# Kernel tuning notes

Hardware: AMD Instinct MI355X
Metric: run time of the kernel (lower is better)

Reference implementation:

```python
import jax, jax.numpy as jnp
import numpy as np

D_MODEL = 256
N_HEADS = 8
N_LEVELS = 3
N_POINTS = 4
HEAD_DIM = D_MODEL // N_HEADS
SPATIAL_SHAPES = [(80, 80), (40, 40), (20, 20)]
B = 16
LEN_Q = 300
N_TOTAL = sum(h * w for h, w in SPATIAL_SHAPES)  # 8400
N_LP = N_LEVELS * N_POINTS


def setup_inputs() -> dict:
    key = jax.random.key(0)
    ks = jax.random.split(key, 8)
    s = 0.02
    return {
        "query": jax.random.normal(ks[0], (B, LEN_Q, D_MODEL), jnp.float32),
        "reference_points": jax.random.uniform(ks[1], (B, LEN_Q, N_LEVELS, 2), jnp.float32),
        "input_flatten": jax.random.normal(ks[2], (B, N_TOTAL, D_MODEL), jnp.float32),
        "W_off": jax.random.normal(ks[3], (D_MODEL, N_HEADS * N_LP * 2), jnp.float32) * s,
        "b_off": jnp.zeros((N_HEADS * N_LP * 2,), jnp.float32),
        "W_attn": jax.random.normal(ks[4], (D_MODEL, N_HEADS * N_LP), jnp.float32) * s,
        "b_attn": jnp.zeros((N_HEADS * N_LP,), jnp.float32),
        "W_val": jax.random.normal(ks[5], (D_MODEL, D_MODEL), jnp.float32) * s,
        "b_val": jnp.zeros((D_MODEL,), jnp.float32),
        "W_out": jax.random.normal(ks[6], (D_MODEL, D_MODEL), jnp.float32) * s,
        "b_out": jnp.zeros((D_MODEL,), jnp.float32),
    }


def _ms_deform_core(value, sampling_locations, attention_weights):
    # value: (B, n_heads, head_dim, N_total); locations: (B, Lq, H, L, P, 2) in [0,1]
    Bq, Lq = sampling_locations.shape[0], sampling_locations.shape[1]
    BN = Bq * N_HEADS
    grids = 2.0 * sampling_locations - 1.0
    starts = np.cumsum([0] + [h * w for h, w in SPATIAL_SHAPES])
    sampled_levels = []
    for lid, (H, W) in enumerate(SPATIAL_SHAPES):
        val_l = value[..., starts[lid]:starts[lid + 1]]                    # (B,H,hd,HW)
        val_flat = val_l.reshape(BN, HEAD_DIM, H * W).transpose(0, 2, 1)   # (BN,HW,hd)
        g = grids[:, :, :, lid].transpose(0, 2, 1, 3, 4).reshape(BN, Lq, N_POINTS, 2)
        ix = ((g[..., 0] + 1.0) * W - 1.0) / 2.0
        iy = ((g[..., 1] + 1.0) * H - 1.0) / 2.0
        ix0 = jnp.floor(ix).astype(jnp.int32)
        iy0 = jnp.floor(iy).astype(jnp.int32)
        ix1 = ix0 + 1
        iy1 = iy0 + 1
        fx = (ix - ix0.astype(ix.dtype))[..., None]
        fy = (iy - iy0.astype(iy.dtype))[..., None]

        def corner(iyc, ixc):
            valid = ((ixc >= 0) & (ixc < W) & (iyc >= 0) & (iyc < H)).astype(val_flat.dtype)
            idx = (jnp.clip(iyc, 0, H - 1) * W + jnp.clip(ixc, 0, W - 1))
            idx = idx.reshape(BN, Lq * N_POINTS, 1)
            v = jnp.take_along_axis(val_flat, idx, axis=1)
            return v.reshape(BN, Lq, N_POINTS, HEAD_DIM) * valid[..., None]

        v00 = corner(iy0, ix0)
        v01 = corner(iy0, ix1)
        v10 = corner(iy1, ix0)
        v11 = corner(iy1, ix1)
        sampled = ((1 - fx) * (1 - fy)) * v00 + (fx * (1 - fy)) * v01 \
                + ((1 - fx) * fy) * v10 + (fx * fy) * v11
        sampled_levels.append(sampled.transpose(0, 3, 1, 2))               # (BN,hd,Lq,P)
    sv = jnp.stack(sampled_levels, axis=-2).reshape(BN, HEAD_DIM, Lq, N_LP)
    a = attention_weights.transpose(0, 2, 1, 3).reshape(BN, 1, Lq, N_LP)
    out = jnp.sum(sv * a, axis=-1)                                         # (BN,hd,Lq)
    return out.reshape(Bq, D_MODEL, Lq).transpose(0, 2, 1)                 # (B,Lq,D)


def reference(query, reference_points, input_flatten,
              W_off, b_off, W_attn, b_attn, W_val, b_val, W_out, b_out):
    Bq, Lq = query.shape[0], query.shape[1]
    value = input_flatten @ W_val + b_val
    value = value.reshape(Bq, -1, N_HEADS, HEAD_DIM).transpose(0, 2, 3, 1)  # (B,H,hd,N)
    off = (query @ W_off + b_off).reshape(Bq, Lq, N_HEADS, N_LEVELS, N_POINTS, 2)
    attn = jax.nn.softmax((query @ W_attn + b_attn).reshape(Bq, Lq, N_HEADS, N_LP), axis=-1)
    # offset normalizer is (W,H) per level (x first)
    norm = jnp.array([[w, h] for h, w in SPATIAL_SHAPES], jnp.float32)
    loc = reference_points[:, :, None, :, None, :] + off / norm[None, None, None, :, None, :]
    out = _ms_deform_core(value, loc, attn)
    return out @ W_out + b_out
```

## Files before the change

kernel.cpp:

```cpp
#include <hip/hip_runtime.h>
#include <hip/hip_bf16.h>

#define DM 256
#define NH 8
#define HD 32
#define NLV 3
#define NPT 4
#define NLP 12
#define BB 16
#define LQ 300
#define NT 8400
#define MROWS (BB * NT)
#define QROWS (BB * LQ)
#define KP 40

typedef __bf16 bf16x8 __attribute__((ext_vector_type(8)));
typedef __bf16 bf16x4 __attribute__((ext_vector_type(4)));
typedef float  f32x16 __attribute__((ext_vector_type(16)));

__global__ void k_wt(const float* __restrict__ W_val,
                     const float* __restrict__ W_off,
                     const float* __restrict__ W_attn,
                     const float* __restrict__ W_out,
                     __hip_bfloat16* __restrict__ Wt,
                     __hip_bfloat16* __restrict__ Wt2,
                     __hip_bfloat16* __restrict__ Wt3)
{
    const int n = blockIdx.x;
    const int k = threadIdx.x;
    if (n < 256) {
        Wt[(size_t)(k >> 5) * 8192 + n * 32 + (k & 31)] =
            __float2bfloat16(W_val[(size_t)k * 256 + n]);
    } else if (n < 544) {
        const int n2 = n - 256;
        float v = (n2 < 192) ? W_off[(size_t)k * 192 + n2]
                             : W_attn[(size_t)k * 96 + (n2 - 192)];
        Wt2[(size_t)(k >> 5) * 9216 + n2 * 32 + (k & 31)] = __float2bfloat16(v);
    } else {
        const int n3 = n - 544;
        Wt3[(size_t)(k >> 5) * 8192 + n3 * 32 + (k & 31)] =
            __float2bfloat16(W_out[(size_t)k * 256 + n3]);
    }
}

__global__ __launch_bounds__(256) void k_valproj(
    const float* __restrict__ A,
    const __hip_bfloat16* __restrict__ Wt,
    const float* __restrict__ bias,
    __hip_bfloat16* __restrict__ V)
{
    __shared__ __hip_bfloat16 As[2][64 * KP];
    __shared__ __hip_bfloat16 Ws[2][256 * KP];

    const int t    = threadIdx.x;
    const int m0   = blockIdx.x * 64;
    const int wave = t >> 6;
    const int lane = t & 63;
    const int lm   = lane & 31;
    const int lk   = (lane >> 5) * 8;

    f32x16 acc[2][2];
#pragma unroll
    for (int i = 0; i < 2; i++)
#pragma unroll
        for (int j = 0; j < 2; j++)
#pragma unroll
            for (int e = 0; e < 16; e++) acc[i][j][e] = 0.f;

    const int ar = t >> 2;
    const int ak = (t & 3) * 8;

    float4 a0, a1;
    bf16x8 w0, w1, w2, w3;

    {
        const float* ap = A + (size_t)(m0 + ar) * 256 + ak;
        a0 = *(const float4*)ap;
        a1 = *(const float4*)(ap + 4);
        const __hip_bfloat16* wp = Wt + t * 32;
        w0 = *(const bf16x8*)(wp + 0);
        w1 = *(const bf16x8*)(wp + 8);
        w2 = *(const bf16x8*)(wp + 16);
        w3 = *(const bf16x8*)(wp + 24);
    }
    {
        union { __hip_bfloat162 h2[4]; bf16x8 v; } ua;
        ua.h2[0] = __float22bfloat162_rn(make_float2(a0.x, a0.y));
        ua.h2[1] = __float22bfloat162_rn(make_float2(a0.z, a0.w));
        ua.h2[2] = __float22bfloat162_rn(make_float2(a1.x, a1.y));
        ua.h2[3] = __float22bfloat162_rn(make_float2(a1.z, a1.w));
        *(bf16x8*)(&As[0][ar * KP + ak]) = ua.v;
        __hip_bfloat16* wd = &Ws[0][t * KP];
        *(bf16x8*)(wd + 0)  = w0;
        *(bf16x8*)(wd + 8)  = w1;
        *(bf16x8*)(wd + 16) = w2;
        *(bf16x8*)(wd + 24) = w3;
    }
    __syncthreads();

    for (int it = 0; it < 8; ++it) {
        float4 na0, na1;
        bf16x8 nw0, nw1, nw2, nw3;
        if (it < 7) {
            const int kt = (it + 1) * 32;
            const float* ap = A + (size_t)(m0 + ar) * 256 + kt + ak;
            na0 = *(const float4*)ap;
            na1 = *(const float4*)(ap + 4);
            const __hip_bfloat16* wp = Wt + (size_t)(it + 1) * 8192 + t * 32;
            nw0 = *(const bf16x8*)(wp + 0);
            nw1 = *(const bf16x8*)(wp + 8);
            nw2 = *(const bf16x8*)(wp + 16);
            nw3 = *(const bf16x8*)(wp + 24);
        }
        const int buf = it & 1;
#pragma unroll
        for (int kk = 0; kk < 32; kk += 16) {
            bf16x8 af0 = *(const bf16x8*)(&As[buf][(0 * 32 + lm) * KP + kk + lk]);
            bf16x8 af1 = *(const bf16x8*)(&As[buf][(1 * 32 + lm) * KP + kk + lk]);
            bf16x8 bf0 = *(const bf16x8*)(&Ws[buf][(wave * 64 + 0 * 32 + lm) * KP + kk + lk]);
            bf16x8 bf1 = *(const bf16x8*)(&Ws[buf][(wave * 64 + 1 * 32 + lm) * KP + kk + lk]);
            acc[0][0] = __builtin_amdgcn_mfma_f32_32x32x16_bf16(af0, bf0, acc[0][0], 0, 0, 0);
            acc[0][1] = __builtin_amdgcn_mfma_f32_32x32x16_bf16(af0, bf1, acc[0][1], 0, 0, 0);
            acc[1][0] = __builtin_amdgcn_mfma_f32_32x32x16_bf16(af1, bf0, acc[1][0], 0, 0, 0);
            acc[1][1] = __builtin_amdgcn_mfma_f32_32x32x16_bf16(af1, bf1, acc[1][1], 0, 0, 0);
        }
        if (it < 7) {
            union { __hip_bfloat162 h2[4]; bf16x8 v; } ua;
            ua.h2[0] = __float22bfloat162_rn(make_float2(na0.x, na0.y));
            ua.h2[1] = __float22bfloat162_rn(make_float2(na0.z, na0.w));
            ua.h2[2] = __float22bfloat162_rn(make_float2(na1.x, na1.y));
            ua.h2[3] = __float22bfloat162_rn(make_float2(na1.z, na1.w));
            const int nb = buf ^ 1;
            *(bf16x8*)(&As[nb][ar * KP + ak]) = ua.v;
            __hip_bfloat16* wd = &Ws[nb][t * KP];
            *(bf16x8*)(wd + 0)  = nw0;
            *(bf16x8*)(wd + 8)  = nw1;
            *(bf16x8*)(wd + 16) = nw2;
            *(bf16x8*)(wd + 24) = nw3;
            __syncthreads();
        }
    }

#pragma unroll
    for (int ni = 0; ni < 2; ni++) {
        const int n  = wave * 64 + ni * 32 + lm;
        const float bn = bias[n];
        const int h  = n >> 5;
        const int d  = n & 31;
#pragma unroll
        for (int mi = 0; mi < 2; mi++) {
#pragma unroll
            for (int r = 0; r < 16; r++) {
                int rl = (r & 3) + 8 * (r >> 2) + 4 * (lane >> 5);
                int m  = m0 + mi * 32 + rl;
                int b  = m / NT;
                int pos = m - b * NT;
                V[((size_t)(b * NH + h) * NT + pos) * HD + d] =
                    __float2bfloat16(acc[mi][ni][r] + bn);
            }
        }
    }
}

__global__ __launch_bounds__(192) void k_offattn(
    const float* __restrict__ Q,
    const __hip_bfloat16* __restrict__ Wt2,
    const float* __restrict__ boff,
    const float* __restrict__ battn,
    float* __restrict__ off_out,
    float* __restrict__ attn_out)
{
    __shared__ __hip_bfloat16 As[32 * KP];
    __shared__ __hip_bfloat16 Ws[288 * KP];

    const int t    = threadIdx.x;
    const int m0   = blockIdx.x * 32;
    const int wave = t >> 6;
    const int lane = t & 63;
    const int lm   = lane & 31;
    const int lk   = (lane >> 5) * 8;

    f32x16 acc[3];
#pragma unroll
    for (int j = 0; j < 3; j++)
#pragma unroll
        for (int e = 0; e < 16; e++) acc[j][e] = 0.f;

    for (int kt = 0; kt < 256; kt += 32) {
        if (t < 128) {
            const int ar = t >> 2;
            const int ak = (t & 3) * 8;
            const float* ap = Q + (size_t)(m0 + ar) * 256 + kt + ak;
            float4 a0 = *(const float4*)ap;
            float4 a1 = *(const float4*)(ap + 4);
            union { __hip_bfloat162 h2[4]; bf16x8 v; } ua;
            ua.h2[0] = __float22bfloat162_rn(make_float2(a0.x, a0.y));
            ua.h2[1] = __float22bfloat162_rn(make_float2(a0.z, a0.w));
            ua.h2[2] = __float22bfloat162_rn(make_float2(a1.x, a1.y));
            ua.h2[3] = __float22bfloat162_rn(make_float2(a1.z, a1.w));
            *(bf16x8*)(As + ar * KP + ak) = ua.v;
        }
        {
            const __hip_bfloat16* wp = Wt2 + (size_t)(kt >> 5) * 9216 + t * 32;
            __hip_bfloat16* wd = Ws + t * KP;
            *(bf16x8*)(wd + 0)  = *(const bf16x8*)(wp + 0);
            *(bf16x8*)(wd + 8)  = *(const bf16x8*)(wp + 8);
            *(bf16x8*)(wd + 16) = *(const bf16x8*)(wp + 16);
            *(bf16x8*)(wd + 24) = *(const bf16x8*)(wp + 24);
            if (t < 96) {
                const __hip_bfloat16* wp2 = Wt2 + (size_t)(kt >> 5) * 9216 + (t + 192) * 32;
                __hip_bfloat16* wd2 = Ws + (t + 192) * KP;
                *(bf16x8*)(wd2 + 0)  = *(const bf16x8*)(wp2 + 0);
                *(bf16x8*)(wd2 + 8)  = *(const bf16x8*)(wp2 + 8);
                *(bf16x8*)(wd2 + 16) = *(const bf16x8*)(wp2 + 16);
                *(bf16x8*)(wd2 + 24) = *(const bf16x8*)(wp2 + 24);
            }
        }
        __syncthreads();

#pragma unroll
        for (int kk = 0; kk < 32; kk += 16) {
            bf16x8 af = *(const bf16x8*)(As + lm * KP + kk + lk);
#pragma unroll
            for (int j = 0; j < 3; j++) {
                bf16x8 bf = *(const bf16x8*)(Ws + (wave * 96 + j * 32 + lm) * KP + kk + lk);
                acc[j] = __builtin_amdgcn_mfma_f32_32x32x16_bf16(af, bf, acc[j], 0, 0, 0);
            }
        }
        __syncthreads();
    }

#pragma unroll
    for (int j = 0; j < 3; j++) {
        const int n = wave * 96 + j * 32 + lm;
        const float bias_ = (n < 192) ? boff[n] : battn[n - 192];
#pragma unroll
        for (int r = 0; r < 16; r++) {
            int rl = (r & 3) + 8 * (r >> 2) + 4 * (lane >> 5);
            int m  = m0 + rl;
            float v = acc[j][r] + bias_;
            if (n < 192) off_out[(size_t)m * 192 + n] = v;
            else         attn_out[(size_t)m * 96 + (n - 192)] = v;
        }
    }
}

__global__ __launch_bounds__(256) void k_sample(
    const float* __restrict__ off_raw,
    const float* __restrict__ attn_raw,
    const float* __restrict__ refp,
    const __hip_bfloat16* __restrict__ V,
    __hip_bfloat16* __restrict__ sampled)
{
    const int t  = threadIdx.x;
    const int q2 = t >> 7;
    const int tq = t & 127;
    const int bq = blockIdx.x * 2 + q2;
    const int b  = bq / LQ;

    __shared__ float aw[2][96];
    __shared__ float wc[2][96][4];
    __shared__ int   ic[2][96][4];

    if (tq < 8) {
        float v[12];
        float mx = -1e30f;
#pragma unroll
        for (int i = 0; i < 12; i++) {
            v[i] = attn_raw[(size_t)bq * 96 + tq * 12 + i];
            mx = fmaxf(mx, v[i]);
        }
        float s = 0.f;
#pragma unroll
        for (int i = 0; i < 12; i++) { v[i] = expf(v[i] - mx); s += v[i]; }
        float inv = 1.f / s;
#pragma unroll
        for (int i = 0; i < 12; i++) aw[q2][tq * 12 + i] = v[i] * inv;
    }
    __syncthreads();

    if (tq < 96) {
        const float dims[3]  = {80.f, 40.f, 20.f};
        const int startsl[3] = {0, 6400, 8000};
        const int idiml[3]   = {80, 40, 20};
        int h = tq / 12, lp = tq - h * 12, l = lp >> 2, p = lp & 3;
        float ox = off_raw[(size_t)bq * 192 + ((h * 3 + l) * 4 + p) * 2 + 0];
        float oy = off_raw[(size_t)bq * 192 + ((h * 3 + l) * 4 + p) * 2 + 1];
        float rx = refp[(size_t)bq * 6 + l * 2 + 0];
        float ry = refp[(size_t)bq * 6 + l * 2 + 1];
        float D  = dims[l];
        float lx = rx + ox / D;
        float ly = ry + oy / D;
        float ix = lx * D - 0.5f;
        float iy = ly * D - 0.5f;
        const int Dl = idiml[l];
        const int st = startsl[l];

        float fix = floorf(ix), fiy = floorf(iy);
        int ix0 = (int)fix, iy0 = (int)fiy;
        int ix1 = ix0 + 1, iy1 = iy0 + 1;
        float fx = ix - fix, fy = iy - fiy;

        float mx0 = (ix0 >= 0 && ix0 < Dl) ? 1.f : 0.f;
        float mx1 = (ix1 >= 0 && ix1 < Dl) ? 1.f : 0.f;
        float my0 = (iy0 >= 0 && iy0 < Dl) ? 1.f : 0.f;
        float my1 = (iy1 >= 0 && iy1 < Dl) ? 1.f : 0.f;

        int cx0 = min(max(ix0, 0), Dl - 1);
        int cx1 = min(max(ix1, 0), Dl - 1);
        int cy0 = min(max(iy0, 0), Dl - 1);
        int cy1 = min(max(iy1, 0), Dl - 1);

        float a = aw[q2][tq];
        wc[q2][tq][0] = (1.f - fx) * (1.f - fy) * mx0 * my0 * a;
        wc[q2][tq][1] = fx * (1.f - fy) * mx1 * my0 * a;
        wc[q2][tq][2] = (1.f - fx) * fy * mx0 * my1 * a;
        wc[q2][tq][3] = fx * fy * mx1 * my1 * a;
        ic[q2][tq][0] = (st + cy0 * Dl + cx0) * HD;
        ic[q2][tq][1] = (st + cy0 * Dl + cx1) * HD;
        ic[q2][tq][2] = (st + cy1 * Dl + cx0) * HD;
        ic[q2][tq][3] = (st + cy1 * Dl + cx1) * HD;
    }
    __syncthreads();

    const int h  = tq >> 4;
    const int dp = (tq & 15) * 2;
    const __hip_bfloat16* vb = V + (size_t)(b * NH + h) * NT * HD + dp;

    float acc0 = 0.f, acc1 = 0.f;
#pragma unroll
    for (int lp = 0; lp < 12; lp++) {
        const int s = h * 12 + lp;
        float4 w4 = *(const float4*)(&wc[q2][s][0]);
        int4   i4 = *(const int4*)(&ic[q2][s][0]);
        float2 v00 = __bfloat1622float2(*(const __hip_bfloat162*)(vb + i4.x));
        float2 v01 = __bfloat1622float2(*(const __hip_bfloat162*)(vb + i4.y));
        float2 v10 = __bfloat1622float2(*(const __hip_bfloat162*)(vb + i4.z));
        float2 v11 = __bfloat1622float2(*(const __hip_bfloat162*)(vb + i4.w));
        acc0 = fmaf(w4.x, v00.x, fmaf(w4.y, v01.x, fmaf(w4.z, v10.x, fmaf(w4.w, v11.x, acc0))));
        acc1 = fmaf(w4.x, v00.y, fmaf(w4.y, v01.y, fmaf(w4.z, v10.y, fmaf(w4.w, v11.y, acc1))));
    }
    *(__hip_bfloat162*)(sampled + (size_t)bq * 256 + h * 32 + dp) =
        __float22bfloat162_rn(make_float2(acc0, acc1));
}

__global__ __launch_bounds__(256) void k_outproj(
    const __hip_bfloat16* __restrict__ A,
    const __hip_bfloat16* __restrict__ Wt3,
    const float* __restrict__ bias,
    float* __restrict__ out)
{
    __shared__ __hip_bfloat16 As[32 * KP];
    __shared__ __hip_bfloat16 Ws[256 * KP];

    const int t    = threadIdx.x;
    const int m0   = blockIdx.x * 32;
    const int wave = t >> 6;
    const int lane = t & 63;
    const int lm   = lane & 31;
    const int lk   = (lane >> 5) * 8;

    f32x16 acc[2];
#pragma unroll
    for (int j = 0; j < 2; j++)
#pragma unroll
        for (int e = 0; e < 16; e++) acc[j][e] = 0.f;

    const int ar = t >> 3;
    const int ak = (t & 7) * 4;

    for (int kt = 0; kt < 256; kt += 32) {
        *(bf16x4*)(As + ar * KP + ak) =
            *(const bf16x4*)(A + (size_t)(m0 + ar) * 256 + kt + ak);
        {
            const __hip_bfloat16* wp = Wt3 + (size_t)(kt >> 5) * 8192 + t * 32;
            __hip_bfloat16* wd = Ws + t * KP;
            *(bf16x8*)(wd + 0)  = *(const bf16x8*)(wp + 0);
            *(bf16x8*)(wd + 8)  = *(const bf16x8*)(wp + 8);
            *(bf16x8*)(wd + 16) = *(const bf16x8*)(wp + 16);
            *(bf16x8*)(wd + 24) = *(const bf16x8*)(wp + 24);
        }
        __syncthreads();

#pragma unroll
        for (int kk = 0; kk < 32; kk += 16) {
            bf16x8 af = *(const bf16x8*)(As + lm * KP + kk + lk);
            bf16x8 bf0 = *(const bf16x8*)(Ws + (wave * 64 + 0 * 32 + lm) * KP + kk + lk);
            bf16x8 bf1 = *(const bf16x8*)(Ws + (wave * 64 + 1 * 32 + lm) * KP + kk + lk);
            acc[0] = __builtin_amdgcn_mfma_f32_32x32x16_bf16(af, bf0, acc[0], 0, 0, 0);
            acc[1] = __builtin_amdgcn_mfma_f32_32x32x16_bf16(af, bf1, acc[1], 0, 0, 0);
        }
        __syncthreads();
    }

#pragma unroll
    for (int j = 0; j < 2; j++) {
        const int n = wave * 64 + j * 32 + lm;
        const float bn = bias[n];
#pragma unroll
        for (int r = 0; r < 16; r++) {
            int rl = (r & 3) + 8 * (r >> 2) + 4 * (lane >> 5);
            int m  = m0 + rl;
            out[(size_t)m * 256 + n] = acc[j][r] + bn;
        }
    }
}

extern "C" void kernel_launch(void* const* d_in, const int* in_sizes, int n_in,
                              void* d_out, int out_size, void* d_ws, size_t ws_size,
                              hipStream_t stream) {
    const float* query  = (const float*)d_in[0];
    const float* refp   = (const float*)d_in[1];
    const float* inputf = (const float*)d_in[2];
    const float* W_off  = (const float*)d_in[3];
    const float* b_off  = (const float*)d_in[4];
    const float* W_attn = (const float*)d_in[5];
    const float* b_attn = (const float*)d_in[6];
    const float* W_val  = (const float*)d_in[7];
    const float* b_val  = (const float*)d_in[8];
    const float* W_out  = (const float*)d_in[9];
    const float* b_out  = (const float*)d_in[10];
    float* out = (float*)d_out;

    char* ws = (char*)d_ws;
    __hip_bfloat16* value   = (__hip_bfloat16*)ws;
    float* off_raw          = (float*)(ws + 68812800);
    float* attn_raw         = (float*)(ws + 72499200);
    __hip_bfloat16* sampled = (__hip_bfloat16*)(ws + 74342400);
    __hip_bfloat16* Wt      = (__hip_bfloat16*)(ws + 76800000);
    __hip_bfloat16* Wt2     = (__hip_bfloat16*)(ws + 76931072);
    __hip_bfloat16* Wt3     = (__hip_bfloat16*)(ws + 77078528);

    k_wt<<<800, 256, 0, stream>>>(W_val, W_off, W_attn, W_out, Wt, Wt2, Wt3);
    k_valproj<<<MROWS / 64, 256, 0, stream>>>(inputf, Wt, b_val, value);
    k_offattn<<<QROWS / 32, 192, 0, stream>>>(query, Wt2, b_off, b_attn,
                                              off_raw, attn_raw);
    k_sample<<<QROWS / 2, 256, 0, stream>>>(off_raw, attn_raw, refp, value, sampled);
    k_outproj<<<QROWS / 32, 256, 0, stream>>>(sampled, Wt3, b_out, out);
}
```

Before: 283.4 us.

## Restructure value projection GEMM to 32-row tiles with single-buffered K=64 stages

The value-projection kernel now handles 32 rows per block instead of 64, launching twice as many blocks. It also drops the register-prefetch double buffering in favour of a single LDS buffer that stages K in chunks of 64 with two barriers per chunk. The smaller per-block footprint is meant to raise occupancy and parallelism. In exchange, each block reuses the weight tile across fewer rows, so weight loads into LDS double, and global load latency is no longer overlapped with MFMA work.

```diff
diff --git a/kernel.cpp b/kernel.cpp
--- a/kernel.cpp
+++ b/kernel.cpp
@@ -13,6 +13,7 @@
 #define MROWS (BB * NT)
 #define QROWS (BB * LQ)
 #define KP 40
+#define KP2 72
 
 typedef __bf16 bf16x8 __attribute__((ext_vector_type(8)));
 typedef __bf16 bf16x4 __attribute__((ext_vector_type(4)));
@@ -49,115 +50,78 @@
     const float* __restrict__ bias,
     __hip_bfloat16* __restrict__ V)
 {
-    __shared__ __hip_bfloat16 As[2][64 * KP];
-    __shared__ __hip_bfloat16 Ws[2][256 * KP];
+    __shared__ __hip_bfloat16 As[32 * KP2];
+    __shared__ __hip_bfloat16 Ws[256 * KP2];
 
     const int t    = threadIdx.x;
-    const int m0   = blockIdx.x * 64;
+    const int m0   = blockIdx.x * 32;
     const int wave = t >> 6;
     const int lane = t & 63;
     const int lm   = lane & 31;
     const int lk   = (lane >> 5) * 8;
 
-    f32x16 acc[2][2];
-#pragma unroll
-    for (int i = 0; i < 2; i++)
-#pragma unroll
-        for (int j = 0; j < 2; j++)
-#pragma unroll
-            for (int e = 0; e < 16; e++) acc[i][j][e] = 0.f;
-
-    const int ar = t >> 2;
-    const int ak = (t & 3) * 8;
-
-    float4 a0, a1;
-    bf16x8 w0, w1, w2, w3;
-
-    {
-        const float* ap = A + (size_t)(m0 + ar) * 256 + ak;
-        a0 = *(const float4*)ap;
-        a1 = *(const float4*)(ap + 4);
-        const __hip_bfloat16* wp = Wt + t * 32;
-        w0 = *(const bf16x8*)(wp + 0);
-        w1 = *(const bf16x8*)(wp + 8);
-        w2 = *(const bf16x8*)(wp + 16);
-        w3 = *(const bf16x8*)(wp + 24);
-    }
-    {
-        union { __hip_bfloat162 h2[4]; bf16x8 v; } ua;
-        ua.h2[0] = __float22bfloat162_rn(make_float2(a0.x, a0.y));
-        ua.h2[1] = __float22bfloat162_rn(make_float2(a0.z, a0.w));
-        ua.h2[2] = __float22bfloat162_rn(make_float2(a1.x, a1.y));
-        ua.h2[3] = __float22bfloat162_rn(make_float2(a1.z, a1.w));
-        *(bf16x8*)(&As[0][ar * KP + ak]) = ua.v;
-        __hip_bfloat16* wd = &Ws[0][t * KP];
-        *(bf16x8*)(wd + 0)  = w0;
-        *(bf16x8*)(wd + 8)  = w1;
-        *(bf16x8*)(wd + 16) = w2;
-        *(bf16x8*)(wd + 24) = w3;
-    }
-    __syncthreads();
-
-    for (int it = 0; it < 8; ++it) {
-        float4 na0, na1;
-        bf16x8 nw0, nw1, nw2, nw3;
-        if (it < 7) {
-            const int kt = (it + 1) * 32;
+    f32x16 acc[2];
+#pragma unroll
+    for (int j = 0; j < 2; j++)
+#pragma unroll
+        for (int e = 0; e < 16; e++) acc[j][e] = 0.f;
+
+    const int ar = t >> 3;
+    const int ak = (t & 7) * 8;
+
+    for (int kt = 0; kt < 256; kt += 64) {
+        {
             const float* ap = A + (size_t)(m0 + ar) * 256 + kt + ak;
-            na0 = *(const float4*)ap;
-            na1 = *(const float4*)(ap + 4);
-            const __hip_bfloat16* wp = Wt + (size_t)(it + 1) * 8192 + t * 32;
-            nw0 = *(const bf16x8*)(wp + 0);
-            nw1 = *(const bf16x8*)(wp + 8);
-            nw2 = *(const bf16x8*)(wp + 16);
-            nw3 = *(const bf16x8*)(wp + 24);
-        }
-        const int buf = it & 1;
-#pragma unroll
-        for (int kk = 0; kk < 32; kk += 16) {
-            bf16x8 af0 = *(const bf16x8*)(&As[buf][(0 * 32 + lm) * KP + kk + lk]);
-            bf16x8 af1 = *(const bf16x8*)(&As[buf][(1 * 32 + lm) * KP + kk + lk]);
-            bf16x8 bf0 = *(const bf16x8*)(&Ws[buf][(wave * 64 + 0 * 32 + lm) * KP + kk + lk]);
-            bf16x8 bf1 = *(const bf16x8*)(&Ws[buf][(wave * 64 + 1 * 32 + lm) * KP + kk + lk]);
-            acc[0][0] = __builtin_amdgcn_mfma_f32_32x32x16_bf16(af0, bf0, acc[0][0], 0, 0, 0);
-            acc[0][1] = __builtin_amdgcn_mfma_f32_32x32x16_bf16(af0, bf1, acc[0][1], 0, 0, 0);
-            acc[1][0] = __builtin_amdgcn_mfma_f32_32x32x16_bf16(af1, bf0, acc[1][0], 0, 0, 0);
-            acc[1][1] = __builtin_amdgcn_mfma_f32_32x32x16_bf16(af1, bf1, acc[1][1], 0, 0, 0);
-        }
-        if (it < 7) {
+            float4 a0 = *(const float4*)ap;
+            float4 a1 = *(const float4*)(ap + 4);
             union { __hip_bfloat162 h2[4]; bf16x8 v; } ua;
-            ua.h2[0] = __float22bfloat162_rn(make_float2(na0.x, na0.y));
-            ua.h2[1] = __float22bfloat162_rn(make_float2(na0.z, na0.w));
-            ua.h2[2] = __float22bfloat162_rn(make_float2(na1.x, na1.y));
-            ua.h2[3] = __float22bfloat162_rn(make_float2(na1.z, na1.w));
-            const int nb = buf ^ 1;
-            *(bf16x8*)(&As[nb][ar * KP + ak]) = ua.v;
-            __hip_bfloat16* wd = &Ws[nb][t * KP];
-            *(bf16x8*)(wd + 0)  = nw0;
-            *(bf16x8*)(wd + 8)  = nw1;
-            *(bf16x8*)(wd + 16) = nw2;
-            *(bf16x8*)(wd + 24) = nw3;
-            __syncthreads();
-        }
-    }
-
-#pragma unroll
-    for (int ni = 0; ni < 2; ni++) {
-        const int n  = wave * 64 + ni * 32 + lm;
+            ua.h2[0] = __float22bfloat162_rn(make_float2(a0.x, a0.y));
+            ua.h2[1] = __float22bfloat162_rn(make_float2(a0.z, a0.w));
+            ua.h2[2] = __float22bfloat162_rn(make_float2(a1.x, a1.y));
+            ua.h2[3] = __float22bfloat162_rn(make_float2(a1.z, a1.w));
+            *(bf16x8*)(As + ar * KP2 + ak) = ua.v;
+        }
+        {
+            const int kt5 = kt >> 5;
+            const __hip_bfloat16* wp0 = Wt + (size_t)kt5 * 8192 + t * 32;
+            const __hip_bfloat16* wp1 = wp0 + 8192;
+            __hip_bfloat16* wd = Ws + t * KP2;
+            *(bf16x8*)(wd + 0)  = *(const bf16x8*)(wp0 + 0);
+            *(bf16x8*)(wd + 8)  = *(const bf16x8*)(wp0 + 8);
+            *(bf16x8*)(wd + 16) = *(const bf16x8*)(wp0 + 16);
+            *(bf16x8*)(wd + 24) = *(const bf16x8*)(wp0 + 24);
+            *(bf16x8*)(wd + 32) = *(const bf16x8*)(wp1 + 0);
+            *(bf16x8*)(wd + 40) = *(const bf16x8*)(wp1 + 8);
+            *(bf16x8*)(wd + 48) = *(const bf16x8*)(wp1 + 16);
+            *(bf16x8*)(wd + 56) = *(const bf16x8*)(wp1 + 24);
+        }
+        __syncthreads();
+
+#pragma unroll
+        for (int kk = 0; kk < 64; kk += 16) {
+            bf16x8 af  = *(const bf16x8*)(As + lm * KP2 + kk + lk);
+            bf16x8 bf0 = *(const bf16x8*)(Ws + (wave * 64 + lm) * KP2 + kk + lk);
+            bf16x8 bf1 = *(const bf16x8*)(Ws + (wave * 64 + 32 + lm) * KP2 + kk + lk);
+            acc[0] = __builtin_amdgcn_mfma_f32_32x32x16_bf16(af, bf0, acc[0], 0, 0, 0);
+            acc[1] = __builtin_amdgcn_mfma_f32_32x32x16_bf16(af, bf1, acc[1], 0, 0, 0);
+        }
+        __syncthreads();
+    }
+
+#pragma unroll
+    for (int j = 0; j < 2; j++) {
+        const int n  = wave * 64 + j * 32 + lm;
         const float bn = bias[n];
         const int h  = n >> 5;
         const int d  = n & 31;
 #pragma unroll
-        for (int mi = 0; mi < 2; mi++) {
-#pragma unroll
-            for (int r = 0; r < 16; r++) {
-                int rl = (r & 3) + 8 * (r >> 2) + 4 * (lane >> 5);
-                int m  = m0 + mi * 32 + rl;
-                int b  = m / NT;
-                int pos = m - b * NT;
-                V[((size_t)(b * NH + h) * NT + pos) * HD + d] =
-                    __float2bfloat16(acc[mi][ni][r] + bn);
-            }
+        for (int r = 0; r < 16; r++) {
+            int rl = (r & 3) + 8 * (r >> 2) + 4 * (lane >> 5);
+            int m  = m0 + rl;
+            int b  = m / NT;
+            int pos = m - b * NT;
+            V[((size_t)(b * NH + h) * NT + pos) * HD + d] =
+                __float2bfloat16(acc[j][r] + bn);
         }
     }
 }
@@ -432,7 +396,7 @@
     __hip_bfloat16* Wt3     = (__hip_bfloat16*)(ws + 77078528);
 
     k_wt<<<800, 256, 0, stream>>>(W_val, W_off, W_attn, W_out, Wt, Wt2, Wt3);
-    k_valproj<<<MROWS / 64, 256, 0, stream>>>(inputf, Wt, b_val, value);
+    k_valproj<<<MROWS / 32, 256, 0, stream>>>(inputf, Wt, b_val, value);
     k_offattn<<<QROWS / 32, 192, 0, stream>>>(query, Wt2, b_off, b_attn,
                                               off_raw, attn_raw);
     k_sample<<<QROWS / 2, 256, 0, stream>>>(off_raw, attn_raw, refp, value, sampled);
```

New measurement: 288.1 us. About the same (+1.7%).
